# Kernel tuning notes

Measured on AMD Instinct MI355X. Metric: run time of the kernel, lower is better.

Reference implementation:

```python
import jax, jax.numpy as jnp
import numpy as np

N = 24  # input_size
TRIL = N * (N + 1) // 2  # 300
_rows, _cols = np.tril_indices(N)  # row-major order, matches torch.tril_indices


def setup_inputs() -> dict:
    key = jax.random.key(0)
    ks = jax.random.split(key, 8)
    B = 131072
    x = jax.random.normal(ks[0], (B, N), dtype=jnp.float32)
    # MLP params: Linear(N,128), Linear(128,32), Linear(32,TRIL)
    def lin(k, fan_in, fan_out):
        k1, k2 = jax.random.split(k)
        lim = 1.0 / np.sqrt(fan_in)
        W = jax.random.uniform(k1, (fan_out, fan_in), jnp.float32, -lim, lim)
        b = jax.random.uniform(k2, (fan_out,), jnp.float32, -lim, lim)
        return W, b
    W1, b1 = lin(ks[1], N, 128)
    W2, b2 = lin(ks[2], 128, 32)
    W3, b3 = lin(ks[3], 32, TRIL)
    return {"x": x, "W1": W1, "b1": b1, "W2": W2, "b2": b2, "W3": W3, "b3": b3}


def reference(x, W1, b1, W2, b2, W3, b3):
    # MLP: Linear -> ELU -> Linear -> ELU -> Linear -> Softplus
    h = jax.nn.elu(x @ W1.T + b1)           # [B,128]
    h = jax.nn.elu(h @ W2.T + b2)           # [B,32]
    c = jax.nn.softplus(h @ W3.T + b3)      # [B,TRIL]
    B = x.shape[0]
    # scatter into lower-triangular Cholesky factor
    L = jnp.zeros((B, N, N), dtype=x.dtype).at[:, _rows, _cols].set(c)  # [B,N,N]
    A = jnp.einsum('bij,bkj->bik', L, L)    # C @ C^T, SPD
    y = jnp.einsum('bi,bij,bj->b', x, A, x)[:, None]  # quadratic form, [B,1]
    return y
```

## Files before the change

### kernel.cpp

```cpp
#include <hip/hip_runtime.h>
#include <hip/hip_bf16.h>
#include <math.h>


constexpr int NI  = 24;
constexpr int H1  = 128;
constexpr int H2  = 32;
constexpr int SPB = 64;
constexpr int NT_TOT = 19;
constexpr int W3R = 304;
constexpr float LOG2E = 1.4426950408889634f;
constexpr float LN2SQ = 0.4804530139182014f;

typedef __attribute__((ext_vector_type(8))) short bf16x8;
typedef __attribute__((ext_vector_type(4))) float f32x4;

struct TriMap { unsigned char i[320]; unsigned char j[320]; };
constexpr TriMap mk_map() {
    TriMap m{};
    int t = 0;
    for (int i = 0; i < NI; ++i)
        for (int j = 0; j <= i; ++j) { m.i[t] = (unsigned char)i; m.j[t] = (unsigned char)j; ++t; }
    for (; t < 320; ++t) { m.i[t] = 0; m.j[t] = 0; }
    return m;
}
constexpr TriMap TM = mk_map();

__device__ __forceinline__ float elu_f(float v) {
    return v > 0.0f ? v : __expf(v) - 1.0f;
}
__device__ __forceinline__ float exp2_hw(float x) {
    float r; asm("v_exp_f32 %0, %1" : "=v"(r) : "v"(x)); return r;
}
__device__ __forceinline__ float log2_hw(float x) {
    float r; asm("v_log_f32 %0, %1" : "=v"(r) : "v"(x)); return r;
}
__device__ __forceinline__ float softplus_g(float zp) {
    return fmaxf(zp, 0.0f) + log2_hw(1.0f + exp2_hw(-fabsf(zp)));
}
__device__ __forceinline__ unsigned short f2bf(float f) {
    return __builtin_bit_cast(unsigned short, __float2bfloat16(f));
}
__device__ __forceinline__ unsigned int pk2(float a, float b) {
    return (unsigned int)f2bf(a) | ((unsigned int)f2bf(b) << 16);
}
__device__ __forceinline__ bf16x8 cvt8(const float* __restrict__ p) {
    float4 a = *reinterpret_cast<const float4*>(p);
    float4 b = *reinterpret_cast<const float4*>(p + 4);
    uint4 u = make_uint4(pk2(a.x, a.y), pk2(a.z, a.w), pk2(b.x, b.y), pk2(b.z, b.w));
    return __builtin_bit_cast(bf16x8, u);
}

__global__ void wcvt(const float* __restrict__ W1, const float* __restrict__ W2,
                     const float* __restrict__ W3, const float* __restrict__ b3,
                     unsigned short* __restrict__ ws) {
    int idx = blockIdx.x * 256 + threadIdx.x;
    if (idx < 4096) {
        int n = idx >> 5, k = idx & 31;
        ws[idx] = f2bf(k < NI ? W1[n * NI + k] : 0.0f);
    } else if (idx < 8192) {
        ws[idx] = f2bf(W2[idx - 4096]);
    } else if (idx < 8192 + W3R * H2) {
        int j = idx - 8192;
        int t = j >> 5;
        ws[idx] = f2bf(t < 300 ? W3[j] * LOG2E : 0.0f);
    } else if (idx < 8192 + W3R * H2 + W3R) {
        int t = idx - (8192 + W3R * H2);
        float* b3s = reinterpret_cast<float*>(ws + 17920);
        b3s[t] = (t < 300) ? b3[t] * LOG2E : 0.0f;
    }
}


template<int CH, int W>
__device__ __forceinline__ void consume4(const unsigned int* __restrict__ crow,
                                         const float xr[NI], float v[6]) {
    #pragma unroll
    for (int tl = 0; tl < 32; ++tl) {
        const int t = CH * 32 + tl;
        if (t < 300) {
            const int j = TM.j[t];
            if ((j & 7) == W || (j & 7) == (7 - W)) {
                const int slot = 2 * (j >> 3) + (((j & 7) == W) ? 0 : 1);
                unsigned int u = crow[(CH & 1) * 16 + (tl >> 1)];
                unsigned int bits = (tl & 1) ? (u & 0xffff0000u) : (u << 16);
                float cv = __builtin_bit_cast(float, bits);
                v[slot] = fmaf(xr[TM.i[t]], cv, v[slot]);
            }
        }
    }
}

__global__ __launch_bounds__(256, 8) void qnet_fused(
    const float* __restrict__ x,
    const unsigned short* __restrict__ w1b, const float* __restrict__ b1,
    const unsigned short* __restrict__ w2b, const float* __restrict__ b2,
    const unsigned short* __restrict__ w3b, const float* __restrict__ b3s,
    float* __restrict__ y, int B)
{
    __shared__ __align__(16) unsigned char L[15104];
    unsigned short* h2b = reinterpret_cast<unsigned short*>(L);
    unsigned short* h1s = reinterpret_cast<unsigned short*>(L + 5120);
    unsigned int*   cbw = reinterpret_cast<unsigned int*>(L + 5120);
    float*          vx  = reinterpret_cast<float*>(L + 5120);

    const int tid  = threadIdx.x;
    const int lane = tid & 63;
    const int lr   = lane & 15, lq = lane >> 4;
    const int w    = __builtin_amdgcn_readfirstlane(tid >> 6);
    const size_t sbase = (size_t)blockIdx.x * SPB;

    float xr[NI];
    {
        const float4* xp4 = reinterpret_cast<const float4*>(x + (sbase + lane) * NI);
        #pragma unroll
        for (int q = 0; q < NI / 4; ++q) {
            float4 t4 = xp4[q];
            xr[4*q+0] = t4.x; xr[4*q+1] = t4.y; xr[4*q+2] = t4.z; xr[4*q+3] = t4.w;
        }
    }

    const int srow = w * 16 + lr;
    bf16x8 xf = cvt8(x + (sbase + srow) * NI + (lq == 3 ? 0 : lq * 8));

    f32x4 acc[2];
    acc[0] = (f32x4){0.f, 0.f, 0.f, 0.f};
    acc[1] = (f32x4){0.f, 0.f, 0.f, 0.f};

    #pragma unroll
    for (int kk = 0; kk < 4; ++kk) {
        #pragma unroll
        for (int n = 0; n < 2; ++n) {
            const int nt1 = 2 * kk + n;
            bf16x8 af = *reinterpret_cast<const bf16x8*>(w1b + (nt1 * 16 + lr) * 32 + lq * 8);
            const float4 bb1 = *reinterpret_cast<const float4*>(b1 + nt1 * 16 + 4 * lq);
            f32x4 a = {0.f, 0.f, 0.f, 0.f};
            a = __builtin_amdgcn_mfma_f32_16x16x32_bf16(af, xf, a, 0, 0, 0);
            unsigned int p0 = pk2(elu_f(a[0] + bb1.x), elu_f(a[1] + bb1.y));
            unsigned int p1 = pk2(elu_f(a[2] + bb1.z), elu_f(a[3] + bb1.w));
            unsigned long long pw = (unsigned long long)p0 | ((unsigned long long)p1 << 32);
            *reinterpret_cast<unsigned long long*>(
                h1s + srow * 40 + n * 16 + 4 * lq) = pw;
        }
        bf16x8 hb = *reinterpret_cast<const bf16x8*>(h1s + srow * 40 + lq * 8);
        #pragma unroll
        for (int n2 = 0; n2 < 2; ++n2) {
            bf16x8 wf = *reinterpret_cast<const bf16x8*>(
                w2b + (n2 * 16 + lr) * H1 + kk * 32 + lq * 8);
            acc[n2] = __builtin_amdgcn_mfma_f32_16x16x32_bf16(wf, hb, acc[n2], 0, 0, 0);
        }
    }

    #pragma unroll
    for (int n2 = 0; n2 < 2; ++n2) {
        const float4 bb2 = *reinterpret_cast<const float4*>(b2 + n2 * 16 + 4 * lq);
        unsigned int p0 = pk2(elu_f(acc[n2][0] + bb2.x), elu_f(acc[n2][1] + bb2.y));
        unsigned int p1 = pk2(elu_f(acc[n2][2] + bb2.z), elu_f(acc[n2][3] + bb2.w));
        unsigned long long pw = (unsigned long long)p0 | ((unsigned long long)p1 << 32);
        *reinterpret_cast<unsigned long long*>(
            h2b + srow * 40 + n2 * 16 + 4 * lq) = pw;
    }
    __syncthreads();

    float v[6];
    #pragma unroll
    for (int q = 0; q < 6; ++q) v[q] = 0.f;

    const int nt_off = w >> 1;
    const int st0 = 2 * (w & 1);

#define QNET_CHUNK(CH)                                                         \
    {                                                                          \
        const int my_nt = 2 * (CH) + nt_off;                                   \
        if (my_nt < NT_TOT) {                                                  \
            bf16x8 af = *reinterpret_cast<const bf16x8*>(                      \
                w3b + (my_nt * 16 + lr) * H2 + lq * 8);                        \
            const float4 b4 = *reinterpret_cast<const float4*>(                \
                b3s + my_nt * 16 + 4 * lq);                                    \
            _Pragma("unroll")                                                  \
            for (int u = 0; u < 2; ++u) {                                      \
                const int st = st0 + u;                                        \
                bf16x8 hb = *reinterpret_cast<const bf16x8*>(                  \
                    h2b + (st * 16 + lr) * 40 + lq * 8);                       \
                f32x4 a = {0.f, 0.f, 0.f, 0.f};                                \
                a = __builtin_amdgcn_mfma_f32_16x16x32_bf16(af, hb, a, 0, 0, 0);\
                float s0 = softplus_g(a[0] + b4.x);                            \
                float s1 = softplus_g(a[1] + b4.y);                            \
                float s2 = softplus_g(a[2] + b4.z);                            \
                float s3 = softplus_g(a[3] + b4.w);                            \
                const int word = (st * 16 + lr) * 39 + ((CH) & 1) * 16         \
                                 + nt_off * 8 + 2 * lq;                        \
                cbw[word]     = pk2(s0, s1);                                   \
                cbw[word + 1] = pk2(s2, s3);                                   \
            }                                                                  \
        }                                                                      \
        __syncthreads();                                                       \
        const unsigned int* crow = cbw + lane * 39;                            \
        if      (w == 0) consume4<(CH), 0>(crow, xr, v);                       \
        else if (w == 1) consume4<(CH), 1>(crow, xr, v);                       \
        else if (w == 2) consume4<(CH), 2>(crow, xr, v);                       \
        else             consume4<(CH), 3>(crow, xr, v);                       \
    }

    QNET_CHUNK(0) QNET_CHUNK(1) QNET_CHUNK(2) QNET_CHUNK(3) QNET_CHUNK(4)
    QNET_CHUNK(5) QNET_CHUNK(6) QNET_CHUNK(7) QNET_CHUNK(8) QNET_CHUNK(9)
#undef QNET_CHUNK

    float py = 0.f;
    #pragma unroll
    for (int q = 0; q < 6; ++q) py = fmaf(v[q], v[q], py);

    __syncthreads();
    if (w > 0) vx[lane * 4 + (w - 1)] = py;
    __syncthreads();
    if (w == 0) {
        float tot = py + vx[lane * 4 + 0] + vx[lane * 4 + 1] + vx[lane * 4 + 2];
        y[sbase + lane] = LN2SQ * tot;
    }
}

extern "C" void kernel_launch(void* const* d_in, const int* in_sizes, int n_in,
                              void* d_out, int out_size, void* d_ws, size_t ws_size,
                              hipStream_t stream) {
    const float* x  = (const float*)d_in[0];
    const float* W1 = (const float*)d_in[1];
    const float* b1 = (const float*)d_in[2];
    const float* W2 = (const float*)d_in[3];
    const float* b2 = (const float*)d_in[4];
    const float* W3 = (const float*)d_in[5];
    const float* b3 = (const float*)d_in[6];
    float* y = (float*)d_out;

    unsigned short* ws = (unsigned short*)d_ws;
    const unsigned short* w1b = ws;
    const unsigned short* w2b = ws + 4096;
    const unsigned short* w3b = ws + 8192;
    const float* b3s = reinterpret_cast<const float*>(ws + 17920);

    const int B = in_sizes[0] / NI;
    const int cvt_elems = 8192 + W3R * H2 + W3R;
    wcvt<<<dim3((cvt_elems + 255) / 256), dim3(256), 0, stream>>>(W1, W2, W3, b3, ws);
    qnet_fused<<<dim3(B / SPB), dim3(256), 0, stream>>>(
        x, w1b, b1, w2b, b2, w3b, b3s, y, B);
}
```

Measured before the change: 41.13 us.

## Stage x and softplus outputs in fp32 LDS, change column ownership per wave

Each wave now loads a slice of x into shared memory instead of every thread keeping all 24 x values in registers. The softplus outputs of the third layer are stored as fp32 in LDS rather than packed bf16, so the bf16 unpack work goes away. The quadratic-form columns are redistributed so each wave owns the columns with j mod 4 equal to its index. This lowers register pressure and ALU work at the cost of more LDS traffic, larger shared memory, and an extra barrier per chunk.

Measured after the change: 38.68 us. -6.0%, faster.

```diff
diff --git a/kernel.cpp b/kernel.cpp
--- a/kernel.cpp
+++ b/kernel.cpp
@@ -13,6 +13,7 @@
 constexpr float LN2SQ = 0.4804530139182014f;
 
 typedef __attribute__((ext_vector_type(8))) short bf16x8;
+typedef __attribute__((ext_vector_type(2))) float f32x2;
 typedef __attribute__((ext_vector_type(4))) float f32x4;
 
 struct TriMap { unsigned char i[320]; unsigned char j[320]; };
@@ -71,23 +72,15 @@
     }
 }
 
-
 template<int CH, int W>
-__device__ __forceinline__ void consume4(const unsigned int* __restrict__ crow,
-                                         const float xr[NI], float v[6]) {
+__device__ __forceinline__ void consume5(const float* __restrict__ crow,
+                                         const float* __restrict__ xrow,
+                                         float v[6]) {
     #pragma unroll
     for (int tl = 0; tl < 32; ++tl) {
         const int t = CH * 32 + tl;
-        if (t < 300) {
-            const int j = TM.j[t];
-            if ((j & 7) == W || (j & 7) == (7 - W)) {
-                const int slot = 2 * (j >> 3) + (((j & 7) == W) ? 0 : 1);
-                unsigned int u = crow[(CH & 1) * 16 + (tl >> 1)];
-                unsigned int bits = (tl & 1) ? (u & 0xffff0000u) : (u << 16);
-                float cv = __builtin_bit_cast(float, bits);
-                v[slot] = fmaf(xr[TM.i[t]], cv, v[slot]);
-            }
-        }
+        if (t < 300 && (TM.j[t] & 3) == W)
+            v[TM.j[t] >> 2] = fmaf(xrow[TM.i[t]], crow[tl], v[TM.j[t] >> 2]);
     }
 }
 
@@ -98,11 +91,12 @@
     const unsigned short* __restrict__ w3b, const float* __restrict__ b3s,
     float* __restrict__ y, int B)
 {
-    __shared__ __align__(16) unsigned char L[15104];
-    unsigned short* h2b = reinterpret_cast<unsigned short*>(L);
-    unsigned short* h1s = reinterpret_cast<unsigned short*>(L + 5120);
-    unsigned int*   cbw = reinterpret_cast<unsigned int*>(L + 5120);
-    float*          vx  = reinterpret_cast<float*>(L + 5120);
+    __shared__ __align__(16) unsigned char L[20224];
+    float*          xs  = reinterpret_cast<float*>(L);
+    unsigned short* h2b = reinterpret_cast<unsigned short*>(L + 6400);
+    unsigned short* h1s = reinterpret_cast<unsigned short*>(L + 11520);
+    float*          cb  = reinterpret_cast<float*>(L + 11520);
+    float*          vx  = reinterpret_cast<float*>(L + 11520);
 
     const int tid  = threadIdx.x;
     const int lane = tid & 63;
@@ -110,14 +104,14 @@
     const int w    = __builtin_amdgcn_readfirstlane(tid >> 6);
     const size_t sbase = (size_t)blockIdx.x * SPB;
 
-    float xr[NI];
     {
-        const float4* xp4 = reinterpret_cast<const float4*>(x + (sbase + lane) * NI);
-        #pragma unroll
-        for (int q = 0; q < NI / 4; ++q) {
-            float4 t4 = xp4[q];
-            xr[4*q+0] = t4.x; xr[4*q+1] = t4.y; xr[4*q+2] = t4.z; xr[4*q+3] = t4.w;
-        }
+        const float* xp = x + (sbase + lane) * NI + 6 * w;
+        f32x2 a = *reinterpret_cast<const f32x2*>(xp);
+        f32x2 b = *reinterpret_cast<const f32x2*>(xp + 2);
+        f32x2 c = *reinterpret_cast<const f32x2*>(xp + 4);
+        float* dst = xs + lane * 25 + 6 * w;
+        dst[0] = a[0]; dst[1] = a[1]; dst[2] = b[0];
+        dst[3] = b[1]; dst[4] = c[0]; dst[5] = c[1];
     }
 
     const int srow = w * 16 + lr;
@@ -184,22 +178,27 @@
                     h2b + (st * 16 + lr) * 40 + lq * 8);                       \
                 f32x4 a = {0.f, 0.f, 0.f, 0.f};                                \
                 a = __builtin_amdgcn_mfma_f32_16x16x32_bf16(af, hb, a, 0, 0, 0);\
-                float s0 = softplus_g(a[0] + b4.x);                            \
-                float s1 = softplus_g(a[1] + b4.y);                            \
-                float s2 = softplus_g(a[2] + b4.z);                            \
-                float s3 = softplus_g(a[3] + b4.w);                            \
-                const int word = (st * 16 + lr) * 39 + ((CH) & 1) * 16         \
-                                 + nt_off * 8 + 2 * lq;                        \
-                cbw[word]     = pk2(s0, s1);                                   \
-                cbw[word + 1] = pk2(s2, s3);                                   \
+                       \
+                f32x2 w0, w1;                                                  \
+                w0[0] = softplus_g(a[0] + b4.x);                               \
+                w0[1] = softplus_g(a[1] + b4.y);                               \
+                w1[0] = softplus_g(a[2] + b4.z);                               \
+                w1[1] = softplus_g(a[3] + b4.w);                               \
+                float* dst = cb + (st * 16 + lr) * 34 + nt_off * 16 + 4 * lq;  \
+                *reinterpret_cast<f32x2*>(dst)     = w0;                       \
+                *reinterpret_cast<f32x2*>(dst + 2) = w1;                       \
             }                                                                  \
         }                                                                      \
         __syncthreads();                                                       \
-        const unsigned int* crow = cbw + lane * 39;                            \
-        if      (w == 0) consume4<(CH), 0>(crow, xr, v);                       \
-        else if (w == 1) consume4<(CH), 1>(crow, xr, v);                       \
-        else if (w == 2) consume4<(CH), 2>(crow, xr, v);                       \
-        else             consume4<(CH), 3>(crow, xr, v);                       \
+        {                                                                      \
+            const float* crow = cb + lane * 34;                                \
+            const float* xrow = xs + lane * 25;                                \
+            if      (w == 0) consume5<(CH), 0>(crow, xrow, v);                 \
+            else if (w == 1) consume5<(CH), 1>(crow, xrow, v);                 \
+            else if (w == 2) consume5<(CH), 2>(crow, xrow, v);                 \
+            else             consume5<(CH), 3>(crow, xrow, v);                 \
+        }                                                                      \
+        __syncthreads();                                                       \
     }
 
     QNET_CHUNK(0) QNET_CHUNK(1) QNET_CHUNK(2) QNET_CHUNK(3) QNET_CHUNK(4)
@@ -210,11 +209,10 @@
     #pragma unroll
     for (int q = 0; q < 6; ++q) py = fmaf(v[q], v[q], py);
 
-    __syncthreads();
-    if (w > 0) vx[lane * 4 + (w - 1)] = py;
+    if (w > 0) vx[lane * 3 + (w - 1)] = py;
     __syncthreads();
     if (w == 0) {
-        float tot = py + vx[lane * 4 + 0] + vx[lane * 4 + 1] + vx[lane * 4 + 2];
+        float tot = py + vx[lane * 3 + 0] + vx[lane * 3 + 1] + vx[lane * 3 + 2];
         y[sbase + lane] = LN2SQ * tot;
     }
 }
```
